# Optimization experiments

Measured on AMD Instinct MI355X. Metric: run time of the kernel, lower is better.

Reference implementation:

```python
import jax, jax.numpy as jnp
import numpy as np

WINDOW = 32
CHUNK = 16


def _z_indices(size: int) -> np.ndarray:
    # Faithful port of VisualRetina._precompute_z (Morton/Z-order permutation).
    y = np.repeat(np.arange(size), size)
    x = np.tile(np.arange(size), size)
    z = np.zeros_like(y)
    for i in range(8):
        z |= ((x & (1 << i)) << i) | ((y & (1 << i)) << (i + 1))
    # z values are unique for size<=256, so argsort order is unambiguous
    return np.argsort(z)


def setup_inputs() -> dict:
    key = jax.random.key(0)
    x = jax.random.normal(key, (256, 3, 224, 224), dtype=jnp.float32)
    return {"x": x}


def reference(x):
    B, C, H, W = x.shape
    ws = WINDOW
    # F.interpolate default mode='nearest': src_idx = floor(dst_idx * in/out)
    ih = (jnp.arange(ws) * H) // ws
    iw = (jnp.arange(ws) * W) // ws
    x_resized = x[:, :, ih, :][:, :, :, iw]              # [B,C,32,32]

    zi = jnp.asarray(_z_indices(ws))                      # [1024] fixed permutation
    x_flat = x_resized.reshape(B, C, ws * ws)
    x_z = x_flat[:, :, zi]                                # Z-order gather

    num_chunks = (ws * ws) // CHUNK                       # 64
    chunks = x_z.reshape(B, C, num_chunks, CHUNK)

    t = jnp.linspace(-1.0, 1.0, CHUNK)
    T_mat = jnp.stack([t ** 3, t ** 2, t, jnp.ones_like(t)], axis=1)  # [16,4]
    T_pinv = jnp.linalg.pinv(T_mat)                       # [4,16]

    y = jnp.transpose(chunks, (0, 2, 3, 1))               # [B,nc,16,C]
    coeffs = jnp.einsum('kt,bntc->bnkc', T_pinv, y)       # [B,nc,4,C]
    y_pred = jnp.einsum('tk,bnkc->bntc', T_mat, coeffs)   # [B,nc,16,C]

    residuals = jnp.mean((y - y_pred) ** 2, axis=2)       # [B,nc,C]
    sigma = jnp.sqrt(residuals)[:, :, None, :]            # [B,nc,1,C]

    token_data = jnp.concatenate([coeffs, sigma], axis=2) # [B,nc,5,C]
    structure = token_data.mean(axis=-1)                  # [B,nc,5]
    return structure[:, :, None, :]                       # [B,nc,1,5]
```

## Files before the change

### kernel.cpp

```cpp
#include <hip/hip_runtime.h>


#define BATCH 256
#define NCHUNK 64
#define HW 224

__global__ __launch_bounds__(64) void retina_kernel(const float* __restrict__ x,
                                                    float* __restrict__ out) {
    int tid = blockIdx.x * blockDim.x + threadIdx.x;
    if (tid >= BATCH * NCHUNK) return;
    int b = tid >> 6;
    int n = tid & 63;
    int xh = (n & 1) | ((n >> 1) & 2) | ((n >> 2) & 4);
    int yh = ((n >> 1) & 1) | ((n >> 2) & 2) | ((n >> 3) & 4);
    const float* __restrict__ xb = x + (size_t)b * 3 * HW * HW;

    float s0[3] = {0.f, 0.f, 0.f};
    float s1[3] = {0.f, 0.f, 0.f};
    float s2[3] = {0.f, 0.f, 0.f};
    float s3[3] = {0.f, 0.f, 0.f};
    float sq[3] = {0.f, 0.f, 0.f};

#pragma unroll
    for (int t = 0; t < 16; ++t) {
        int dx = (t & 1) | ((t >> 1) & 2);
        int dy = ((t >> 1) & 1) | ((t >> 2) & 2);
        int h = 7 * (4 * yh + dy);
        int w = 7 * (4 * xh + dx);
        int off = h * HW + w;
        float tt = -1.0f + (2.0f / 15.0f) * (float)t;
        float t2 = tt * tt;
        float t3 = t2 * tt;
#pragma unroll
        for (int c = 0; c < 3; ++c) {
            float v = xb[c * (HW * HW) + off];
            s0[c] += v;
            s1[c] += tt * v;
            s2[c] += t2 * v;
            s3[c] += t3 * v;
            sq[c] += v * v;
        }
    }

    const float S0f = 16.0f;
    const float S2f = 1360.0f / 225.0f;
    const float S4f = 206992.0f / 50625.0f;
    const float S6f = 37308880.0f / 11390625.0f;
    const float inv_det_odd  = 1.0f / (S6f * S2f - S4f * S4f);
    const float inv_det_even = 1.0f / (S4f * S0f - S2f * S2f);

    float m0 = 0.f, m1 = 0.f, m2 = 0.f, m3 = 0.f, ms = 0.f;
#pragma unroll
    for (int c = 0; c < 3; ++c) {
        float a_cube = (S2f * s3[c] - S4f * s1[c]) * inv_det_odd;
        float a_lin  = (S6f * s1[c] - S4f * s3[c]) * inv_det_odd;
        float a_quad = (S0f * s2[c] - S2f * s0[c]) * inv_det_even;
        float a_cons = (S4f * s0[c] - S2f * s2[c]) * inv_det_even;
        float ss = sq[c] - (a_cube * s3[c] + a_quad * s2[c] +
                            a_lin * s1[c] + a_cons * s0[c]);
        float sig = sqrtf(fmaxf(ss, 0.0f) * (1.0f / 16.0f));
        m0 += a_cube; m1 += a_quad; m2 += a_lin; m3 += a_cons; ms += sig;
    }

    float* o = out + (size_t)tid * 5;
    const float third = 1.0f / 3.0f;
    o[0] = m0 * third;
    o[1] = m1 * third;
    o[2] = m2 * third;
    o[3] = m3 * third;
    o[4] = ms * third;
}

extern "C" void kernel_launch(void* const* d_in, const int* in_sizes, int n_in,
                              void* d_out, int out_size, void* d_ws, size_t ws_size,
                              hipStream_t stream) {
    const float* x = (const float*)d_in[0];
    float* out = (float*)d_out;
    int total = BATCH * NCHUNK;
    int block = 64;
    int grid = (total + block - 1) / block;
    retina_kernel<<<grid, block, 0, stream>>>(x, out);
}
```

Before: 185.3 us.

## Stage sampled pixels in shared memory and split chunk fits per channel

Each block now loads an 8-row by 32-column strip of subsampled pixels for all three channels into shared memory, with one load per thread. Then 48 threads each fit one (chunk, channel) cubic, and 16 threads average the three channels and write the tokens. This is meant to raise memory-level parallelism: the old version issued 48 dependent strided loads per thread from only 256 blocks. The cost is two barriers and mostly idle threads in the compute phase. Each load is still a scattered 4-byte access at a stride of 7 elements, so DRAM sector efficiency stays poor.

```diff
diff --git a/kernel.cpp b/kernel.cpp
--- a/kernel.cpp
+++ b/kernel.cpp
@@ -2,73 +2,84 @@
 
 
 #define BATCH 256
-#define NCHUNK 64
 #define HW 224
 
-__global__ __launch_bounds__(64) void retina_kernel(const float* __restrict__ x,
-                                                    float* __restrict__ out) {
-    int tid = blockIdx.x * blockDim.x + threadIdx.x;
-    if (tid >= BATCH * NCHUNK) return;
-    int b = tid >> 6;
-    int n = tid & 63;
-    int xh = (n & 1) | ((n >> 1) & 2) | ((n >> 2) & 4);
-    int yh = ((n >> 1) & 1) | ((n >> 2) & 2) | ((n >> 3) & 4);
+__global__ __launch_bounds__(256) void retina_kernel(const float* __restrict__ x,
+                                                     float* __restrict__ out) {
+    __shared__ float smem[3][8][33];
+    __shared__ float tok[3][16][5];
+
+    int blk = blockIdx.x;
+    int b   = blk >> 2;
+    int yq  = blk & 3;
+    int tid = threadIdx.x;
+
     const float* __restrict__ xb = x + (size_t)b * 3 * HW * HW;
 
-    float s0[3] = {0.f, 0.f, 0.f};
-    float s1[3] = {0.f, 0.f, 0.f};
-    float s2[3] = {0.f, 0.f, 0.f};
-    float s3[3] = {0.f, 0.f, 0.f};
-    float sq[3] = {0.f, 0.f, 0.f};
+    int yl = tid >> 5;
+    int xg = tid & 31;
+    int off = (7 * (8 * yq + yl)) * HW + 7 * xg;
+#pragma unroll
+    for (int c = 0; c < 3; ++c) {
+        smem[c][yl][xg] = xb[c * (HW * HW) + off];
+    }
+    __syncthreads();
 
+    if (tid < 48) {
+        int c   = tid >> 4;
+        int lc  = tid & 15;
+        int xh  = lc & 7;
+        int ylh = lc >> 3;
+
+        float s0 = 0.f, s1 = 0.f, s2 = 0.f, s3 = 0.f, sq = 0.f;
 #pragma unroll
-    for (int t = 0; t < 16; ++t) {
-        int dx = (t & 1) | ((t >> 1) & 2);
-        int dy = ((t >> 1) & 1) | ((t >> 2) & 2);
-        int h = 7 * (4 * yh + dy);
-        int w = 7 * (4 * xh + dx);
-        int off = h * HW + w;
-        float tt = -1.0f + (2.0f / 15.0f) * (float)t;
-        float t2 = tt * tt;
-        float t3 = t2 * tt;
+        for (int t = 0; t < 16; ++t) {
+            int dx = (t & 1) | ((t >> 1) & 2);
+            int dy = ((t >> 1) & 1) | ((t >> 2) & 2);
+            float v = smem[c][4 * ylh + dy][4 * xh + dx];
+            float tt = -1.0f + (2.0f / 15.0f) * (float)t;
+            float t2 = tt * tt;
+            float t3 = t2 * tt;
+            s0 += v; s1 += tt * v; s2 += t2 * v; s3 += t3 * v; sq += v * v;
+        }
+
+        const float S0f = 16.0f;
+        const float S2f = 1360.0f / 225.0f;
+        const float S4f = 206992.0f / 50625.0f;
+        const float S6f = 37308880.0f / 11390625.0f;
+        const float inv_det_odd  = 1.0f / (S6f * S2f - S4f * S4f);
+        const float inv_det_even = 1.0f / (S4f * S0f - S2f * S2f);
+
+        float a_cube = (S2f * s3 - S4f * s1) * inv_det_odd;
+        float a_lin  = (S6f * s1 - S4f * s3) * inv_det_odd;
+        float a_quad = (S0f * s2 - S2f * s0) * inv_det_even;
+        float a_cons = (S4f * s0 - S2f * s2) * inv_det_even;
+        float ss = sq - (a_cube * s3 + a_quad * s2 +
+                         a_lin * s1 + a_cons * s0);
+        float sig = sqrtf(fmaxf(ss, 0.0f) * (1.0f / 16.0f));
+
+        tok[c][lc][0] = a_cube;
+        tok[c][lc][1] = a_quad;
+        tok[c][lc][2] = a_lin;
+        tok[c][lc][3] = a_cons;
+        tok[c][lc][4] = sig;
+    }
+    __syncthreads();
+
+    if (tid < 16) {
+        int lc  = tid;
+        int xh  = lc & 7;
+        int ylh = lc >> 3;
+        int yh  = 2 * yq + ylh;
+        int n = (xh & 1) | ((yh & 1) << 1) | ((xh & 2) << 1) |
+                ((yh & 2) << 2) | ((xh & 4) << 2) | ((yh & 4) << 3);
+        const float third = 1.0f / 3.0f;
+        float* o = out + ((size_t)b * 64 + n) * 5;
 #pragma unroll
-        for (int c = 0; c < 3; ++c) {
-            float v = xb[c * (HW * HW) + off];
-            s0[c] += v;
-            s1[c] += tt * v;
-            s2[c] += t2 * v;
-            s3[c] += t3 * v;
-            sq[c] += v * v;
+        for (int k = 0; k < 5; ++k) {
+            o[k] = (tok[0][lc][k] + tok[1][lc][k] + tok[2][lc][k]) * third;
         }
     }
-
-    const float S0f = 16.0f;
-    const float S2f = 1360.0f / 225.0f;
-    const float S4f = 206992.0f / 50625.0f;
-    const float S6f = 37308880.0f / 11390625.0f;
-    const float inv_det_odd  = 1.0f / (S6f * S2f - S4f * S4f);
-    const float inv_det_even = 1.0f / (S4f * S0f - S2f * S2f);
-
-    float m0 = 0.f, m1 = 0.f, m2 = 0.f, m3 = 0.f, ms = 0.f;
-#pragma unroll
-    for (int c = 0; c < 3; ++c) {
-        float a_cube = (S2f * s3[c] - S4f * s1[c]) * inv_det_odd;
-        float a_lin  = (S6f * s1[c] - S4f * s3[c]) * inv_det_odd;
-        float a_quad = (S0f * s2[c] - S2f * s0[c]) * inv_det_even;
-        float a_cons = (S4f * s0[c] - S2f * s2[c]) * inv_det_even;
-        float ss = sq[c] - (a_cube * s3[c] + a_quad * s2[c] +
-                            a_lin * s1[c] + a_cons * s0[c]);
-        float sig = sqrtf(fmaxf(ss, 0.0f) * (1.0f / 16.0f));
-        m0 += a_cube; m1 += a_quad; m2 += a_lin; m3 += a_cons; ms += sig;
-    }
-
-    float* o = out + (size_t)tid * 5;
-    const float third = 1.0f / 3.0f;
-    o[0] = m0 * third;
-    o[1] = m1 * third;
-    o[2] = m2 * third;
-    o[3] = m3 * third;
-    o[4] = ms * third;
 }
 
 extern "C" void kernel_launch(void* const* d_in, const int* in_sizes, int n_in,
@@ -76,8 +87,7 @@
                               hipStream_t stream) {
     const float* x = (const float*)d_in[0];
     float* out = (float*)d_out;
-    int total = BATCH * NCHUNK;
-    int block = 64;
-    int grid = (total + block - 1) / block;
+    int grid = BATCH * 4;
+    int block = 256;
     retina_kernel<<<grid, block, 0, stream>>>(x, out);
 }
```

Result: no change. 182.6 us (-1.5%).
